# Kernel tuning notes

Hardware: AMD Instinct MI355X
Metric: run time of the kernel (lower is better)

Reference implementation:

```python
import jax, jax.numpy as jnp
import numpy as np
import math

B, T, DIM, NH = 2, 2048, 2048, 16
HD = DIM // NH  # 128


def rotate_half(x):
    h = x.shape[-1] // 2
    return jnp.concatenate([-x[..., h:], x[..., :h]], axis=-1)


def rope_tables(t_len, rot_dim, base=10000.0, dtype=jnp.float32):
    # rot_dim = head_dim; inv_freq has rot_dim//2 entries -> sin/cos [T, rot_dim//2]
    inv_freq = 1.0 / (base ** (jnp.arange(0, rot_dim, 2, dtype=dtype) / rot_dim))
    t = jnp.arange(t_len, dtype=dtype)
    ang = jnp.einsum('i,j->ij', t, inv_freq)  # [T, rot_dim//2]
    return jnp.sin(ang), jnp.cos(ang)


def apply_rope(q, k, sin, cos):
    # Partial RoPE as in source: rotate only the first half of head_dim,
    # using sin/cos of width head_dim//2 matched to that half.
    h = q.shape[-1] // 2
    q1, q2 = q[..., :h], q[..., h:]
    k1, k2 = k[..., :h], k[..., h:]
    sin = sin[None, None]  # [1,1,T,h]
    cos = cos[None, None]
    q1r = q1 * cos + rotate_half(q1) * sin
    k1r = k1 * cos + rotate_half(k1) * sin
    return jnp.concatenate([q1r, q2], axis=-1), jnp.concatenate([k1r, k2], axis=-1)


def setup_inputs() -> dict:
    key = jax.random.key(0)
    ks = jax.random.split(key, 5)
    s = 1.0 / math.sqrt(DIM)
    return {
        'x': jax.random.normal(ks[0], (B, T, DIM), jnp.float32),
        'wq': jax.random.normal(ks[1], (DIM, DIM), jnp.float32) * s,
        'wk': jax.random.normal(ks[2], (DIM, DIM), jnp.float32) * s,
        'wv': jax.random.normal(ks[3], (DIM, DIM), jnp.float32) * s,
        'wo': jax.random.normal(ks[4], (DIM, DIM), jnp.float32) * s,
    }


def reference(x, wq, wk, wv, wo):
    b, t, c = x.shape
    def proj(w):
        return (x @ w.T).reshape(b, t, NH, HD).transpose(0, 2, 1, 3)  # [B,H,T,hd]
    q, k, v = proj(wq), proj(wk), proj(wv)
    sin, cos = rope_tables(t, HD, dtype=x.dtype)
    q, k = apply_rope(q, k, sin, cos)
    att = jnp.einsum('bhqd,bhkd->bhqk', q, k) * (1.0 / math.sqrt(HD))  # [B,H,T,T]
    att = jax.nn.softmax(att, axis=-1)
    y = jnp.einsum('bhqk,bhkd->bhqd', att, v)
    y = y.transpose(0, 2, 1, 3).reshape(b, t, c)
    return y @ wo.T
```

## Files before the change

kernel.cpp:

```cpp
#include <hip/hip_runtime.h>

typedef unsigned short u16;
typedef __attribute__((ext_vector_type(4))) u16 u16x4;
typedef __attribute__((ext_vector_type(8))) __bf16 bf16x8;
typedef __attribute__((ext_vector_type(4))) float f32x4;

#define B_ 2
#define T_ 2048
#define DIM_ 2048
#define NH_ 16
#define HD_ 128

__device__ __forceinline__ u16 f2b(float f) {
  unsigned u = __builtin_bit_cast(unsigned, f);
  u += 0x7fffu + ((u >> 16) & 1u);
  return (u16)(u >> 16);
}
__device__ __forceinline__ float b2f(u16 h) {
  unsigned u = ((unsigned)h) << 16;
  return __builtin_bit_cast(float, u);
}
__device__ __forceinline__ unsigned pack2(float lo, float hi) {
  return (unsigned)f2b(lo) | ((unsigned)f2b(hi) << 16);
}

typedef __attribute__((address_space(1))) void gvoid_t;
typedef __attribute__((address_space(3))) void lvoid_t;
__device__ __forceinline__ void gload16(const void* g, void* l) {
  __builtin_amdgcn_global_load_lds((gvoid_t*)g, (lvoid_t*)l, 16, 0, 0);
}

__global__ __launch_bounds__(256) void cvt_bf16(const float* x, const float* wq,
    const float* wk, const float* wv, const float* wo,
    u16* xb, u16* wqb, u16* wkb, u16* wvb, u16* wob) {
  int ten = blockIdx.y;
  const float* s; u16* d; int n4;
  if (ten == 0)      { s = x;  d = xb;  n4 = 2097152; }
  else if (ten == 1) { s = wq; d = wqb; n4 = 1048576; }
  else if (ten == 2) { s = wk; d = wkb; n4 = 1048576; }
  else if (ten == 3) { s = wv; d = wvb; n4 = 1048576; }
  else               { s = wo; d = wob; n4 = 1048576; }
  int i = blockIdx.x * 256 + threadIdx.x;
  if (i >= n4) return;
  float4 f = ((const float4*)s)[i];
  u16x4 o = { f2b(f.x), f2b(f.y), f2b(f.z), f2b(f.w) };
  ((u16x4*)d)[i] = o;
}

template <typename OutT>
__device__ __forceinline__ void gemm_bt_body(const u16* A, const u16* Bw, OutT* C) {
  constexpr int K = 2048, N = 2048;
  __shared__ u16 As[128 * 32];
  __shared__ u16 Bs[128 * 32];
  const int tid = threadIdx.x;
  const int w = tid >> 6, l = tid & 63, n = l & 15, quad = l >> 4;
  const int row0 = blockIdx.y * 128, col0 = blockIdx.x * 128;
  const int c = w * 64 + l;
  const int rA = c >> 2, kA = (c & 3) * 8;
  const u16* aP1 = A + (size_t)(row0 + rA) * K + kA;
  const u16* aP2 = A + (size_t)(row0 + 64 + rA) * K + kA;
  const u16* bP1 = Bw + (size_t)(col0 + rA) * K + kA;
  const u16* bP2 = Bw + (size_t)(col0 + 64 + rA) * K + kA;
  char* lA1 = (char*)As + (w * 64) * 16;
  char* lA2 = (char*)As + (256 + w * 64) * 16;
  char* lB1 = (char*)Bs + (w * 64) * 16;
  char* lB2 = (char*)Bs + (256 + w * 64) * 16;
  const int wr0 = (w >> 1) * 64, wc0 = (w & 1) * 64;
  f32x4 acc[4][4] = {};
  for (int kt = 0; kt < K; kt += 32) {
    gload16(aP1, lA1); gload16(aP2, lA2);
    gload16(bP1, lB1); gload16(bP2, lB2);
    aP1 += 32; aP2 += 32; bP1 += 32; bP2 += 32;
    __syncthreads();
    bf16x8 af[4], bfr[4];
#pragma unroll
    for (int mb = 0; mb < 4; ++mb)
      af[mb] = *(const bf16x8*)&As[(wr0 + mb * 16 + n) * 32 + quad * 8];
#pragma unroll
    for (int nb = 0; nb < 4; ++nb)
      bfr[nb] = *(const bf16x8*)&Bs[(wc0 + nb * 16 + n) * 32 + quad * 8];
#pragma unroll
    for (int mb = 0; mb < 4; ++mb)
#pragma unroll
      for (int nb = 0; nb < 4; ++nb)
        acc[mb][nb] = __builtin_amdgcn_mfma_f32_16x16x32_bf16(af[mb], bfr[nb], acc[mb][nb], 0, 0, 0);
    __syncthreads();
  }
#pragma unroll
  for (int mb = 0; mb < 4; ++mb)
#pragma unroll
    for (int nb = 0; nb < 4; ++nb)
#pragma unroll
      for (int r = 0; r < 4; ++r) {
        size_t idx = (size_t)(row0 + wr0 + mb * 16 + quad * 4 + r) * N + (col0 + wc0 + nb * 16 + n);
        float v = acc[mb][nb][r];
        if constexpr (sizeof(OutT) == 2) C[idx] = f2b(v); else C[idx] = v;
      }
}

__global__ __launch_bounds__(256) void gemm_qkv(const u16* A, const u16* w0, const u16* w1,
    const u16* w2, u16* c0, u16* c1, u16* c2) {
  const u16* Bw = (blockIdx.z == 0) ? w0 : (blockIdx.z == 1) ? w1 : w2;
  u16* C = (blockIdx.z == 0) ? c0 : (blockIdx.z == 1) ? c1 : c2;
  gemm_bt_body<u16>(A, Bw, C);
}
__global__ __launch_bounds__(256) void gemm_o(const u16* A, const u16* Bw, float* C) {
  gemm_bt_body<float>(A, Bw, C);
}

__global__ __launch_bounds__(256) void rope_k(u16* Qb, u16* Kb) {
  int gid = blockIdx.x * 256 + threadIdx.x;
  int j = gid & 31;
  int h = (gid >> 5) & 15;
  int row = gid >> 9;
  int t = row & (T_ - 1);
  bool isQ = (blockIdx.y == 0);
  u16* base = (isQ ? Qb : Kb) + (size_t)row * DIM_ + h * HD_;
  double f1 = exp2(-(double)j * 0.20762050593045951);
  double f2 = f1 * 0.01;
  const double INV2PI = 0.15915494309189535;
  double r1d = (double)t * f1 * INV2PI; r1d -= floor(r1d);
  double r2d = (double)t * f2 * INV2PI; r2d -= floor(r2d);
  float rv1 = (float)r1d, rv2 = (float)r2d;
  float c1 = __builtin_amdgcn_cosf(rv1), s1 = __builtin_amdgcn_sinf(rv1);
  float c2 = __builtin_amdgcn_cosf(rv2), s2 = __builtin_amdgcn_sinf(rv2);
  float x1 = b2f(base[j]), x2 = b2f(base[j + 32]);
  float scale = isQ ? 0.12751743342408354f : 1.0f;
  base[j]      = f2b((x1 * c1 - x2 * s1) * scale);
  base[j + 32] = f2b((x2 * c2 + x1 * s2) * scale);
  if (isQ) {
    base[j + 64] = f2b(b2f(base[j + 64]) * scale);
    base[j + 96] = f2b(b2f(base[j + 96]) * scale);
  }
}

__global__ __launch_bounds__(256) void transpose_v(const u16* V, u16* Vt) {
  int b = blockIdx.z;
  int t0 = blockIdx.x * 64, c0 = blockIdx.y * 64;
  __shared__ u16 tile[64][72];
  int tid = threadIdx.x;
#pragma unroll
  for (int i = 0; i < 4; ++i) {
    int v = i * 256 + tid;
    int r = v >> 4, c4 = (v & 15) * 4;
    *(u16x4*)&tile[r][c4] = *(const u16x4*)(V + (size_t)(b * T_ + t0 + r) * DIM_ + c0 + c4);
  }
  __syncthreads();
#pragma unroll
  for (int i = 0; i < 4; ++i) {
    int v = i * 256 + tid;
    int d = v >> 4, t4 = (v & 15) * 4;
    u16x4 o = { tile[t4 + 0][d], tile[t4 + 1][d], tile[t4 + 2][d], tile[t4 + 3][d] };
    *(u16x4*)(Vt + (size_t)(b * DIM_ + c0 + d) * T_ + t0 + t4) = o;
  }
}

__global__ __launch_bounds__(256, 2) void attn_k(const u16* Q, const u16* K, const u16* Vt, u16* Y) {
  const int qt = blockIdx.x, bh = blockIdx.y;
  const int b = bh >> 4, h = bh & 15;
  const int tid = threadIdx.x;
  const int w = tid >> 6, l = tid & 63, n = l & 15, quad = l >> 4;
  __shared__ u16 Ks[2][64 * 128];
  __shared__ u16 Vs[2][128 * 64];

  const u16* Qbase = Q + (size_t)(b * T_ + qt * 128 + w * 32) * DIM_ + h * HD_;
  const u16* Kbase = K + (size_t)(b * T_) * DIM_ + h * HD_;
  const u16* Vbase = Vt + (size_t)(b * DIM_ + h * HD_) * T_;

  bf16x8 qf[2][4];
#pragma unroll
  for (int qtile = 0; qtile < 2; ++qtile)
#pragma unroll
    for (int ks = 0; ks < 4; ++ks)
      qf[qtile][ks] = *(const bf16x8*)(Qbase + (size_t)(qtile * 16 + n) * DIM_ + ks * 32 + quad * 8);

  auto stageK = [&](int itn, u16* dst) {
#pragma unroll
    for (int inst = 0; inst < 4; ++inst) {
      int ci = inst * 256 + w * 64 + l;
      int r = ci >> 4, cl = ci & 15;
      int cg = cl ^ (r & 7);
      gload16(Kbase + (size_t)(itn * 64 + r) * DIM_ + cg * 8, (char*)dst + (inst * 256 + w * 64) * 16);
    }
  };
  auto stageV = [&](int itn, u16* dst) {
#pragma unroll
    for (int inst = 0; inst < 4; ++inst) {
      int ci = inst * 256 + w * 64 + l;
      int r = ci >> 3, cl = ci & 7;
      int cg = cl ^ (r & 7);
      gload16(Vbase + (size_t)r * T_ + itn * 64 + cg * 8, (char*)dst + (inst * 256 + w * 64) * 16);
    }
  };

  f32x4 o[2][8] = {};
  float m_r[2] = { -__builtin_inff(), -__builtin_inff() };
  float l_r[2] = { 0.f, 0.f };

  const int shA = ((quad & 1) * 2) * 16 + n;
  const int shB = shA + 16;
  const bool hiTile = (quad >= 2);

  auto iter_body = [&](const u16* Kc, const u16* Vc, u16* Kn, u16* Vn, int itn) {
    __syncthreads();
    if (itn >= 0) { stageK(itn, Kn); stageV(itn, Vn); }

    f32x4 st[2][4] = {};
#pragma unroll
    for (int ks = 0; ks < 4; ++ks) {
      bf16x8 kf[4];
#pragma unroll
      for (int mt = 0; mt < 4; ++mt)
        kf[mt] = *(const bf16x8*)&Kc[(mt * 16 + n) * 128 + (((ks * 4 + quad) ^ (n & 7)) * 8)];
#pragma unroll
      for (int qtile = 0; qtile < 2; ++qtile)
#pragma unroll
        for (int mt = 0; mt < 4; ++mt)
          st[qtile][mt] = __builtin_amdgcn_mfma_f32_16x16x32_bf16(kf[mt], qf[qtile][ks], st[qtile][mt], 0, 0, 0);
    }

    unsigned pk[2][4][2];
#pragma unroll
    for (int qtile = 0; qtile < 2; ++qtile) {
      float mx = -__builtin_inff();
#pragma unroll
      for (int mt = 0; mt < 4; ++mt)
#pragma unroll
        for (int r = 0; r < 4; ++r) mx = fmaxf(mx, st[qtile][mt][r]);
      mx = fmaxf(mx, __shfl_xor(mx, 16, 64));
      mx = fmaxf(mx, __shfl_xor(mx, 32, 64));
      float mo = m_r[qtile];
      float mn = fmaxf(mo, mx);
      float al = __builtin_amdgcn_exp2f(mo - mn);
      float rs = 0.f;
#pragma unroll
      for (int mt = 0; mt < 4; ++mt)
#pragma unroll
        for (int r = 0; r < 4; ++r) {
          float p = __builtin_amdgcn_exp2f(st[qtile][mt][r] - mn);
          st[qtile][mt][r] = p;
          rs += p;
        }
      rs += __shfl_xor(rs, 16, 64);
      rs += __shfl_xor(rs, 32, 64);
      l_r[qtile] = al * l_r[qtile] + rs;
      m_r[qtile] = mn;
#pragma unroll
      for (int mt = 0; mt < 4; ++mt) {
        pk[qtile][mt][0] = pack2(st[qtile][mt][0], st[qtile][mt][1]);
        pk[qtile][mt][1] = pack2(st[qtile][mt][2], st[qtile][mt][3]);
      }
#pragma unroll
      for (int mt = 0; mt < 8; ++mt)
#pragma unroll
        for (int r = 0; r < 4; ++r) o[qtile][mt][r] *= al;
    }

    typedef __attribute__((ext_vector_type(4))) unsigned uint4v;
    uint4v pT[2][2];
#pragma unroll
    for (int qtile = 0; qtile < 2; ++qtile)
#pragma unroll
      for (int ks2 = 0; ks2 < 2; ++ks2)
#pragma unroll
        for (int jj = 0; jj < 4; ++jj) {
          int src = (jj < 2) ? shA : shB;
          unsigned vA = __shfl((int)pk[qtile][ks2 * 2][jj & 1], src, 64);
          unsigned vB = __shfl((int)pk[qtile][ks2 * 2 + 1][jj & 1], src, 64);
          pT[qtile][ks2][jj] = hiTile ? vB : vA;
        }

#pragma unroll
    for (int ks2 = 0; ks2 < 2; ++ks2) {
      bf16x8 vf[8];
#pragma unroll
      for (int mt = 0; mt < 8; ++mt)
        vf[mt] = *(const bf16x8*)&Vc[(mt * 16 + n) * 64 + (((ks2 * 4 + quad) ^ (n & 7)) * 8)];
#pragma unroll
      for (int qtile = 0; qtile < 2; ++qtile) {
        bf16x8 pfrag = __builtin_bit_cast(bf16x8, pT[qtile][ks2]);
#pragma unroll
        for (int mt = 0; mt < 8; ++mt)
          o[qtile][mt] = __builtin_amdgcn_mfma_f32_16x16x32_bf16(vf[mt], pfrag, o[qtile][mt], 0, 0, 0);
      }
    }
  };

  stageK(0, Ks[0]); stageV(0, Vs[0]);
  for (int it = 0; it < 32; it += 2) {
    iter_body(Ks[0], Vs[0], Ks[1], Vs[1], it + 1);
    iter_body(Ks[1], Vs[1], Ks[0], Vs[0], (it + 2 < 32) ? it + 2 : -1);
  }

  u16* Ybase = Y + (size_t)(b * T_ + qt * 128 + w * 32) * DIM_ + h * HD_;
#pragma unroll
  for (int qtile = 0; qtile < 2; ++qtile) {
    float inv = 1.0f / l_r[qtile];
#pragma unroll
    for (int mt = 0; mt < 8; ++mt) {
      u16x4 ov = { f2b(o[qtile][mt][0] * inv), f2b(o[qtile][mt][1] * inv),
                   f2b(o[qtile][mt][2] * inv), f2b(o[qtile][mt][3] * inv) };
      *(u16x4*)(Ybase + (size_t)(qtile * 16 + n) * DIM_ + mt * 16 + quad * 4) = ov;
    }
  }
}

extern "C" void kernel_launch(void* const* d_in, const int* in_sizes, int n_in,
                              void* d_out, int out_size, void* d_ws, size_t ws_size,
                              hipStream_t stream) {
  const float* x  = (const float*)d_in[0];
  const float* wq = (const float*)d_in[1];
  const float* wk = (const float*)d_in[2];
  const float* wv = (const float*)d_in[3];
  const float* wo = (const float*)d_in[4];

  u16* ws  = (u16*)d_ws;
  u16* xb  = ws;
  u16* wqb = xb + 8388608;
  u16* wkb = wqb + 4194304;
  u16* wvb = wkb + 4194304;
  u16* wob = wvb + 4194304;
  u16* qb  = wob + 4194304;
  u16* kb  = qb + 8388608;
  u16* vb  = kb + 8388608;
  u16* vt  = vb + 8388608;
  u16* yb  = vt + 8388608;

  cvt_bf16<<<dim3(8192, 5), 256, 0, stream>>>(x, wq, wk, wv, wo, xb, wqb, wkb, wvb, wob);
  gemm_qkv<<<dim3(16, 32, 3), 256, 0, stream>>>(xb, wqb, wkb, wvb, qb, kb, vb);
  rope_k<<<dim3(8192, 2), 256, 0, stream>>>(qb, kb);
  transpose_v<<<dim3(32, 32, 2), 256, 0, stream>>>(vb, vt);
  attn_k<<<dim3(16, 32), 256, 0, stream>>>(qb, kb, vt, yb);
  gemm_o<<<dim3(16, 32), 256, 0, stream>>>(yb, wob, (float*)d_out);
}
```

Measured before the change: 419.9 us.

## Fuse RoPE and Q scaling into QKV GEMM epilogue, double-buffer and swizzle LDS

Removes the separate RoPE kernel by applying the rotation and the Q softmax scale to the GEMM accumulators before the bf16 store. This avoids an extra read-modify-write pass over Q and K. The GEMM main loop now double-buffers LDS tiles with one barrier per k-step, and the tile layout is XOR-swizzled to reduce bank conflicts. Launch bounds ask for 3 blocks per CU, which may pressure registers, and the epilogue recomputes the sin/cos terms in double precision per element. RoPE now rotates fp32 accumulators before bf16 rounding, so outputs differ slightly from the old path.

```diff
diff --git a/kernel.cpp b/kernel.cpp
--- a/kernel.cpp
+++ b/kernel.cpp
@@ -48,90 +48,91 @@
 }
 
 template <typename OutT>
-__device__ __forceinline__ void gemm_bt_body(const u16* A, const u16* Bw, OutT* C) {
+__device__ __forceinline__ void gemm_body(const u16* A, const u16* Bw, OutT* C,
+                                          int row0, int col0, int rotate, int scaleQ) {
   constexpr int K = 2048, N = 2048;
-  __shared__ u16 As[128 * 32];
-  __shared__ u16 Bs[128 * 32];
+  __shared__ u16 As[2][128 * 32];
+  __shared__ u16 Bs[2][128 * 32];
   const int tid = threadIdx.x;
   const int w = tid >> 6, l = tid & 63, n = l & 15, quad = l >> 4;
-  const int row0 = blockIdx.y * 128, col0 = blockIdx.x * 128;
-  const int c = w * 64 + l;
-  const int rA = c >> 2, kA = (c & 3) * 8;
-  const u16* aP1 = A + (size_t)(row0 + rA) * K + kA;
-  const u16* aP2 = A + (size_t)(row0 + 64 + rA) * K + kA;
-  const u16* bP1 = Bw + (size_t)(col0 + rA) * K + kA;
-  const u16* bP2 = Bw + (size_t)(col0 + 64 + rA) * K + kA;
-  char* lA1 = (char*)As + (w * 64) * 16;
-  char* lA2 = (char*)As + (256 + w * 64) * 16;
-  char* lB1 = (char*)Bs + (w * 64) * 16;
-  char* lB2 = (char*)Bs + (256 + w * 64) * 16;
+  const int r = tid >> 2, cl = tid & 3;
+  const int cg = cl ^ ((r + (r >> 2)) & 3);
+  const u16* aP = A + (size_t)(row0 + r) * K + cg * 8;
+  const u16* bP = Bw + (size_t)(col0 + r) * K + cg * 8;
+  const int ldst = tid * 8;
+  auto stage = [&](int kt, int buf) {
+    gload16(aP + kt, As[buf] + ldst);
+    gload16(aP + kt + (size_t)64 * K, As[buf] + 2048 + ldst);
+    gload16(bP + kt, Bs[buf] + ldst);
+    gload16(bP + kt + (size_t)64 * K, Bs[buf] + 2048 + ldst);
+  };
   const int wr0 = (w >> 1) * 64, wc0 = (w & 1) * 64;
+  const int fsl = (quad ^ ((n + (n >> 2)) & 3)) * 8;
   f32x4 acc[4][4] = {};
+  stage(0, 0);
   for (int kt = 0; kt < K; kt += 32) {
-    gload16(aP1, lA1); gload16(aP2, lA2);
-    gload16(bP1, lB1); gload16(bP2, lB2);
-    aP1 += 32; aP2 += 32; bP1 += 32; bP2 += 32;
+    const int buf = (kt >> 5) & 1;
     __syncthreads();
+    if (kt + 32 < K) stage(kt + 32, buf ^ 1);
     bf16x8 af[4], bfr[4];
 #pragma unroll
     for (int mb = 0; mb < 4; ++mb)
-      af[mb] = *(const bf16x8*)&As[(wr0 + mb * 16 + n) * 32 + quad * 8];
+      af[mb] = *(const bf16x8*)&As[buf][(wr0 + mb * 16 + n) * 32 + fsl];
 #pragma unroll
     for (int nb = 0; nb < 4; ++nb)
-      bfr[nb] = *(const bf16x8*)&Bs[(wc0 + nb * 16 + n) * 32 + quad * 8];
+      bfr[nb] = *(const bf16x8*)&Bs[buf][(wc0 + nb * 16 + n) * 32 + fsl];
 #pragma unroll
     for (int mb = 0; mb < 4; ++mb)
 #pragma unroll
       for (int nb = 0; nb < 4; ++nb)
         acc[mb][nb] = __builtin_amdgcn_mfma_f32_16x16x32_bf16(af[mb], bfr[nb], acc[mb][nb], 0, 0, 0);
-    __syncthreads();
-  }
+  }
+
+  if (rotate && wc0 == 0) {
+#pragma unroll
+    for (int nb = 0; nb < 2; ++nb) {
+      int j = nb * 16 + n;
+      double f1 = exp2(-(double)j * 0.20762050593045951);
+      double f2 = f1 * 0.01;
+      const double INV2PI = 0.15915494309189535;
+#pragma unroll
+      for (int mb = 0; mb < 4; ++mb)
+#pragma unroll
+        for (int rr = 0; rr < 4; ++rr) {
+          int t = (row0 + wr0 + mb * 16 + quad * 4 + rr) & (T_ - 1);
+          double a1 = (double)t * f1 * INV2PI; a1 -= floor(a1);
+          double a2 = (double)t * f2 * INV2PI; a2 -= floor(a2);
+          float c1 = __builtin_amdgcn_cosf((float)a1), s1 = __builtin_amdgcn_sinf((float)a1);
+          float c2 = __builtin_amdgcn_cosf((float)a2), s2 = __builtin_amdgcn_sinf((float)a2);
+          float x1 = acc[mb][nb][rr], x2 = acc[mb][nb + 2][rr];
+          acc[mb][nb][rr]     = x1 * c1 - x2 * s1;
+          acc[mb][nb + 2][rr] = x2 * c2 + x1 * s2;
+        }
+    }
+  }
+  const float osc = scaleQ ? 0.12751743342408354f : 1.0f;
+
 #pragma unroll
   for (int mb = 0; mb < 4; ++mb)
 #pragma unroll
     for (int nb = 0; nb < 4; ++nb)
 #pragma unroll
-      for (int r = 0; r < 4; ++r) {
-        size_t idx = (size_t)(row0 + wr0 + mb * 16 + quad * 4 + r) * N + (col0 + wc0 + nb * 16 + n);
-        float v = acc[mb][nb][r];
+      for (int rr = 0; rr < 4; ++rr) {
+        size_t idx = (size_t)(row0 + wr0 + mb * 16 + quad * 4 + rr) * N + (col0 + wc0 + nb * 16 + n);
+        float v = acc[mb][nb][rr] * osc;
         if constexpr (sizeof(OutT) == 2) C[idx] = f2b(v); else C[idx] = v;
       }
 }
 
-__global__ __launch_bounds__(256) void gemm_qkv(const u16* A, const u16* w0, const u16* w1,
+__global__ __launch_bounds__(256, 3) void gemm_qkv(const u16* A, const u16* w0, const u16* w1,
     const u16* w2, u16* c0, u16* c1, u16* c2) {
-  const u16* Bw = (blockIdx.z == 0) ? w0 : (blockIdx.z == 1) ? w1 : w2;
-  u16* C = (blockIdx.z == 0) ? c0 : (blockIdx.z == 1) ? c1 : c2;
-  gemm_bt_body<u16>(A, Bw, C);
-}
-__global__ __launch_bounds__(256) void gemm_o(const u16* A, const u16* Bw, float* C) {
-  gemm_bt_body<float>(A, Bw, C);
-}
-
-__global__ __launch_bounds__(256) void rope_k(u16* Qb, u16* Kb) {
-  int gid = blockIdx.x * 256 + threadIdx.x;
-  int j = gid & 31;
-  int h = (gid >> 5) & 15;
-  int row = gid >> 9;
-  int t = row & (T_ - 1);
-  bool isQ = (blockIdx.y == 0);
-  u16* base = (isQ ? Qb : Kb) + (size_t)row * DIM_ + h * HD_;
-  double f1 = exp2(-(double)j * 0.20762050593045951);
-  double f2 = f1 * 0.01;
-  const double INV2PI = 0.15915494309189535;
-  double r1d = (double)t * f1 * INV2PI; r1d -= floor(r1d);
-  double r2d = (double)t * f2 * INV2PI; r2d -= floor(r2d);
-  float rv1 = (float)r1d, rv2 = (float)r2d;
-  float c1 = __builtin_amdgcn_cosf(rv1), s1 = __builtin_amdgcn_sinf(rv1);
-  float c2 = __builtin_amdgcn_cosf(rv2), s2 = __builtin_amdgcn_sinf(rv2);
-  float x1 = b2f(base[j]), x2 = b2f(base[j + 32]);
-  float scale = isQ ? 0.12751743342408354f : 1.0f;
-  base[j]      = f2b((x1 * c1 - x2 * s1) * scale);
-  base[j + 32] = f2b((x2 * c2 + x1 * s2) * scale);
-  if (isQ) {
-    base[j + 64] = f2b(b2f(base[j + 64]) * scale);
-    base[j + 96] = f2b(b2f(base[j + 96]) * scale);
-  }
+  const int z = blockIdx.z;
+  const u16* Bw = (z == 0) ? w0 : (z == 1) ? w1 : w2;
+  u16* C = (z == 0) ? c0 : (z == 1) ? c1 : c2;
+  gemm_body<u16>(A, Bw, C, blockIdx.y * 128, blockIdx.x * 128, z < 2, z == 0);
+}
+__global__ __launch_bounds__(256, 3) void gemm_o(const u16* A, const u16* Bw, float* C) {
+  gemm_body<float>(A, Bw, C, blockIdx.y * 128, blockIdx.x * 128, 0, 0);
 }
 
 __global__ __launch_bounds__(256) void transpose_v(const u16* V, u16* Vt) {
@@ -226,7 +227,7 @@
 #pragma unroll
       for (int mt = 0; mt < 4; ++mt)
 #pragma unroll
-        for (int r = 0; r < 4; ++r) mx = fmaxf(mx, st[qtile][mt][r]);
+        for (int r2 = 0; r2 < 4; ++r2) mx = fmaxf(mx, st[qtile][mt][r2]);
       mx = fmaxf(mx, __shfl_xor(mx, 16, 64));
       mx = fmaxf(mx, __shfl_xor(mx, 32, 64));
       float mo = m_r[qtile];
@@ -236,9 +237,9 @@
 #pragma unroll
       for (int mt = 0; mt < 4; ++mt)
 #pragma unroll
-        for (int r = 0; r < 4; ++r) {
-          float p = __builtin_amdgcn_exp2f(st[qtile][mt][r] - mn);
-          st[qtile][mt][r] = p;
+        for (int r2 = 0; r2 < 4; ++r2) {
+          float p = __builtin_amdgcn_exp2f(st[qtile][mt][r2] - mn);
+          st[qtile][mt][r2] = p;
           rs += p;
         }
       rs += __shfl_xor(rs, 16, 64);
@@ -253,7 +254,7 @@
 #pragma unroll
       for (int mt = 0; mt < 8; ++mt)
 #pragma unroll
-        for (int r = 0; r < 4; ++r) o[qtile][mt][r] *= al;
+        for (int r2 = 0; r2 < 4; ++r2) o[qtile][mt][r2] *= al;
     }
 
     typedef __attribute__((ext_vector_type(4))) unsigned uint4v;
@@ -328,7 +329,6 @@
 
   cvt_bf16<<<dim3(8192, 5), 256, 0, stream>>>(x, wq, wk, wv, wo, xb, wqb, wkb, wvb, wob);
   gemm_qkv<<<dim3(16, 32, 3), 256, 0, stream>>>(xb, wqb, wkb, wvb, qb, kb, vb);
-  rope_k<<<dim3(8192, 2), 256, 0, stream>>>(qb, kb);
   transpose_v<<<dim3(32, 32, 2), 256, 0, stream>>>(vb, vt);
   attn_k<<<dim3(16, 32), 256, 0, stream>>>(qb, kb, vt, yb);
   gemm_o<<<dim3(16, 32), 256, 0, stream>>>(yb, wob, (float*)d_out);
```

After: 429.6 us. 2.3% more time.
